# Performance work log

Measured on AMD Instinct MI355X. Metric: run time of the kernel, lower is better.

Reference implementation:

```python
import jax, jax.numpy as jnp
import numpy as np

N, D_IN, E, H, F, T = 50000, 128, 800000, 8, 32, 8
NEG_SLOPE = 0.2


def setup_inputs() -> dict:
    key = jax.random.key(0)
    ks = jax.random.split(key, 12)
    feat = jax.random.normal(ks[0], (N, D_IN), dtype=jnp.float32)
    edge_embeddings = jax.random.normal(ks[1], (E, H), dtype=jnp.float32)
    src = jax.random.randint(ks[2], (E,), 0, N, dtype=jnp.int32)
    dst = jnp.sort(jax.random.randint(ks[3], (E,), 0, N, dtype=jnp.int32))
    etype = jax.random.randint(ks[4], (E,), 0, T, dtype=jnp.int32)
    s = 0.05
    W_src = jax.random.normal(ks[5], (H * F, D_IN), dtype=jnp.float32) * s
    attn_l = jax.random.normal(ks[6], (1, H, F), dtype=jnp.float32) * s
    attn_r = jax.random.normal(ks[7], (1, H, F), dtype=jnp.float32) * s
    attn_e = jax.random.normal(ks[8], (1, H, F), dtype=jnp.float32) * s
    W_e = jax.random.normal(ks[9], (H * F, H), dtype=jnp.float32) * s
    type_emb = jax.random.normal(ks[10], (T, F), dtype=jnp.float32) * s
    k2 = jax.random.split(ks[11], 3)
    W_et = jax.random.normal(k2[0], (H * F, F), dtype=jnp.float32) * s
    attn_et = jax.random.normal(k2[1], (1, H, F), dtype=jnp.float32) * s
    bias = jnp.zeros((H * F,), dtype=jnp.float32)
    return dict(feat=feat, edge_embeddings=edge_embeddings, src=src, dst=dst,
                etype=etype, W_src=W_src, attn_l=attn_l, attn_r=attn_r,
                attn_e=attn_e, W_e=W_e, type_emb=type_emb, W_et=W_et,
                attn_et=attn_et, bias=bias)


def _leaky_relu(x):
    return jnp.where(x >= 0, x, NEG_SLOPE * x)


def reference(feat, edge_embeddings, src, dst, etype, W_src, attn_l, attn_r,
              attn_e, W_e, type_emb, W_et, attn_et, bias):
    n = feat.shape[0]
    # node transform (shared src/dst weights)
    fs = (feat @ W_src.T).reshape(n, H, F)           # [N,H,F]
    el = (fs * attn_l).sum(-1)                        # [N,H]
    er = (fs * attn_r).sum(-1)                        # [N,H]
    e = el[src] + er[dst]                             # [E,H] (u_add_v)
    # edge embedding attention term
    ee = (edge_embeddings @ W_e.T).reshape(-1, H, F)  # [E,H,F]
    e_score = (ee * attn_e).sum(-1)                   # [E,H]
    # edge type embedding attention term
    te = type_emb[etype]                              # [E,F]
    te = (te @ W_et.T).reshape(-1, H, F)              # [E,H,F]
    t_score = (te * attn_et).sum(-1)                  # [E,H]
    attn = e + e_score + t_score                      # attn_agg = sum
    # edge-type frequency normalization
    counts = jnp.bincount(etype, length=T).astype(jnp.float32)
    w = counts.sum() / (T * counts)                   # [T]
    attn = attn * w[etype][:, None]
    attn = _leaky_relu(attn)                          # v2=False -> after agg
    # edge softmax over incoming edges of each dst node
    m = jax.ops.segment_max(attn, dst, num_segments=n)  # [N,H]
    a = jnp.exp(attn - m[dst])
    z = jax.ops.segment_sum(a, dst, num_segments=n)     # [N,H]
    a = a / z[dst]                                      # [E,H]
    # weighted scatter aggregation
    msg = fs[src] * a[:, :, None]                       # [E,H,F]
    out = jax.ops.segment_sum(msg, dst, num_segments=n) # [N,H,F]
    return out + bias.reshape(1, H, F)
```

## Files before the change

kernel.cpp:

```cpp
#include <hip/hip_runtime.h>
#include <math.h>

#define N_NODES 50000
#define D_IN    128
#define E_EDGES 800000
#define H_HEADS 8
#define F_FEAT  32
#define T_TYPES 8
#define HF      256
#define NEG_SLOPE 0.2f
#define HIST_BLOCKS 64
#define GEMM_BLOCKS 391
#define OFF_BLOCKS  196
#define K1_HIST_BASE GEMM_BLOCKS
#define K1_OFF_BASE  (GEMM_BLOCKS + HIST_BLOCKS)
#define K1_TAB       (GEMM_BLOCKS + HIST_BLOCKS + OFF_BLOCKS)
#define K1_GRID      (K1_TAB + 1)
#define NGROUPS      ((N_NODES + 63) / 64)

using short8 = __attribute__((__ext_vector_type__(8))) short;
using f32x4  = __attribute__((__ext_vector_type__(4))) float;

__device__ inline float bf2f(unsigned short u) {
    union { unsigned int i; float f; } v; v.i = ((unsigned int)u) << 16; return v.f;
}
__device__ inline unsigned short f2bf(float f) {
    unsigned int x = __float_as_uint(f);
    unsigned int r = (x + 0x7fffu + ((x >> 16) & 1u)) >> 16;
    return (unsigned short)r;
}
__device__ inline unsigned int pk2bf(float a, float b) {
    return (unsigned int)f2bf(a) | ((unsigned int)f2bf(b) << 16);
}

__global__ __launch_bounds__(256) void prep_kernel(const float* __restrict__ feat,
                                                   const float* __restrict__ W,
                                                   const float* __restrict__ attn_l,
                                                   const float* __restrict__ attn_r,
                                                   const int*   __restrict__ etype,
                                                   const int*   __restrict__ dst,
                                                   const float* __restrict__ attn_e,
                                                   const float* __restrict__ W_e,
                                                   const float* __restrict__ attn_et,
                                                   const float* __restrict__ W_et,
                                                   const float* __restrict__ type_emb,
                                                   unsigned short* __restrict__ fsb,
                                                   float* __restrict__ el,
                                                   float* __restrict__ er,
                                                   int* __restrict__ partials,
                                                   int* __restrict__ off,
                                                   float* __restrict__ M,
                                                   float* __restrict__ ttab) {
    __shared__ unsigned short Wl[HF * D_IN];
    __shared__ int sw[4][8];
    __shared__ float q[8][32];
    const int t = threadIdx.x;

    if (blockIdx.x == K1_TAB) {
        {
            int h = t >> 5, f2 = t & 31;
            float s = 0.f;
#pragma unroll 8
            for (int f = 0; f < F_FEAT; ++f)
                s += attn_et[h * 32 + f] * W_et[(h * 32 + f) * 32 + f2];
            q[h][f2] = s;
        }
        __syncthreads();
        if (t < 64) {
            int h = t >> 3, j = t & 7;
            float m = 0.f;
#pragma unroll 8
            for (int f = 0; f < F_FEAT; ++f)
                m += attn_e[h * 32 + f] * W_e[(h * 32 + f) * 8 + j];
            M[h * 8 + j] = m;
            float tt = 0.f;
#pragma unroll 8
            for (int f2 = 0; f2 < F_FEAT; ++f2)
                tt += type_emb[j * 32 + f2] * q[h][f2];
            ttab[j * 8 + h] = tt;
        }
        return;
    }
    if (blockIdx.x >= K1_OFF_BASE) {
        int n = (blockIdx.x - K1_OFF_BASE) * 256 + t;
        if (n > N_NODES) return;
        int lo = 0, hi = E_EDGES;
        while (lo < hi) {
            int mid = (lo + hi) >> 1;
            if (dst[mid] < n) lo = mid + 1; else hi = mid;
        }
        off[n] = lo;
        return;
    }
    if (blockIdx.x >= K1_HIST_BASE) {
        const int hb = blockIdx.x - K1_HIST_BASE;
        int c[8] = {0,0,0,0,0,0,0,0};
        const int stride = HIST_BLOCKS * 256;
        for (int e = hb * 256 + t; e < E_EDGES; e += stride) {
            int ty = etype[e];
#pragma unroll
            for (int k = 0; k < 8; ++k) c[k] += (ty == k) ? 1 : 0;
        }
#pragma unroll
        for (int k = 0; k < 8; ++k) {
            c[k] += __shfl_xor(c[k], 1);  c[k] += __shfl_xor(c[k], 2);
            c[k] += __shfl_xor(c[k], 4);  c[k] += __shfl_xor(c[k], 8);
            c[k] += __shfl_xor(c[k], 16); c[k] += __shfl_xor(c[k], 32);
        }
        const int wv = t >> 6, l = t & 63;
        if (l == 0) {
#pragma unroll
            for (int k = 0; k < 8; ++k) sw[wv][k] = c[k];
        }
        __syncthreads();
        if (t < 8) partials[hb * 8 + t] = sw[0][t] + sw[1][t] + sw[2][t] + sw[3][t];
        return;
    }

    for (int i = 0; i < 16; ++i) {
        int slot = i * 256 + t;
        int n = slot >> 4, k16 = slot & 15;
        const float* wp = W + (size_t)n * D_IN + k16 * 8;
        float4 w0 = *(const float4*)wp;
        float4 w1 = *(const float4*)(wp + 4);
        union { unsigned int u[4]; short8 s; } ua;
        ua.u[0] = pk2bf(w0.x, w0.y); ua.u[1] = pk2bf(w0.z, w0.w);
        ua.u[2] = pk2bf(w1.x, w1.y); ua.u[3] = pk2bf(w1.z, w1.w);
        int idx = n * D_IN + ((k16 * 8) ^ ((n & 7) << 3));
        *(short8*)&Wl[idx] = ua.s;
    }
    __syncthreads();

    const int wid = t >> 6, l = t & 63;
    const int r16 = l & 15, kq = l >> 4;
    float alv0[8], alv1[8], arv0[8], arv1[8];
#pragma unroll
    for (int h = 0; h < 8; ++h) {
        alv0[h] = attn_l[h * 32 + r16];  alv1[h] = attn_l[h * 32 + 16 + r16];
        arv0[h] = attn_r[h * 32 + r16];  arv1[h] = attn_r[h * 32 + 16 + r16];
    }

    for (int grp = blockIdx.x; grp < NGROUPS; grp += GEMM_BLOCKS) {
        const int node0 = grp * 64 + wid * 16;
        int arow = node0 + r16;
        if (arow >= N_NODES) arow = N_NODES - 1;
        const float* fp = feat + (size_t)arow * D_IN + kq * 8;

        f32x4 acc[16];
#pragma unroll
        for (int i = 0; i < 16; ++i) acc[i] = (f32x4){0.f, 0.f, 0.f, 0.f};

#pragma unroll
        for (int kc = 0; kc < 4; ++kc) {
            float4 a0 = *(const float4*)(fp + kc * 32);
            float4 a1 = *(const float4*)(fp + kc * 32 + 4);
            union { unsigned int u[4]; short8 s; } ua;
            ua.u[0] = pk2bf(a0.x, a0.y); ua.u[1] = pk2bf(a0.z, a0.w);
            ua.u[2] = pk2bf(a1.x, a1.y); ua.u[3] = pk2bf(a1.z, a1.w);
            short8 af = ua.s;
#pragma unroll
            for (int nsub = 0; nsub < 16; ++nsub) {
                int n = nsub * 16 + r16;
                int idx = n * D_IN + ((kc * 32 + kq * 8) ^ ((n & 7) << 3));
                short8 bf = *(short8*)&Wl[idx];
                acc[nsub] = __builtin_amdgcn_mfma_f32_16x16x32_bf16(af, bf, acc[nsub], 0, 0, 0);
            }
        }

        const int nodeb = node0 + kq * 4;
#pragma unroll
        for (int h = 0; h < 8; ++h) {
            float ev[4], rv[4];
#pragma unroll
            for (int g = 0; g < 4; ++g) {
                ev[g] = acc[2 * h][g] * alv0[h] + acc[2 * h + 1][g] * alv1[h];
                rv[g] = acc[2 * h][g] * arv0[h] + acc[2 * h + 1][g] * arv1[h];
            }
#pragma unroll
            for (int g = 0; g < 4; ++g) {
                ev[g] += __shfl_xor(ev[g], 1); ev[g] += __shfl_xor(ev[g], 2);
                ev[g] += __shfl_xor(ev[g], 4); ev[g] += __shfl_xor(ev[g], 8);
                rv[g] += __shfl_xor(rv[g], 1); rv[g] += __shfl_xor(rv[g], 2);
                rv[g] += __shfl_xor(rv[g], 4); rv[g] += __shfl_xor(rv[g], 8);
            }
            if (r16 == 0) {
#pragma unroll
                for (int g = 0; g < 4; ++g) {
                    int nd = nodeb + g;
                    if (nd < N_NODES) {
                        el[nd * 8 + h] = ev[g];
                        er[nd * 8 + h] = rv[g];
                    }
                }
            }
        }
#pragma unroll
        for (int nsub = 0; nsub < 16; ++nsub) {
            int col = nsub * 16 + r16;
#pragma unroll
            for (int g = 0; g < 4; ++g) {
                int nd = nodeb + g;
                if (nd < N_NODES) fsb[(size_t)nd * HF + col] = f2bf(acc[nsub][g]);
            }
        }
    }
}

__global__ __launch_bounds__(256) void edge_kernel(const float* __restrict__ ee,
        const int* __restrict__ src, const int* __restrict__ dst,
        const int* __restrict__ etype, const float* __restrict__ el,
        const float* __restrict__ er, const float* __restrict__ M,
        const float* __restrict__ ttab, const int* __restrict__ partials,
        unsigned short* __restrict__ pexp) {
    __shared__ float sM[64], sT[64], sw[8];
    int t = threadIdx.x;
    if (t < 64) {
        sM[t] = M[t]; sT[t] = ttab[t];
        int j = t & 7, b = t >> 3;
        int c = 0;
#pragma unroll 8
        for (int i = 0; i < HIST_BLOCKS / 8; ++i)
            c += partials[(b + 8 * i) * 8 + j];
        c += __shfl_xor(c, 8); c += __shfl_xor(c, 16); c += __shfl_xor(c, 32);
        if (t < 8) {
            if (c < 1) c = 1;
            sw[t] = (float)E_EDGES / (8.0f * (float)c);
        }
    }
    __syncthreads();
    int e = blockIdx.x * 256 + t;
    if (e >= E_EDGES) return;
    int s = src[e], d = dst[e], ty = etype[e];
    float4 e0 = *(const float4*)&ee[(size_t)e * 8];
    float4 e1 = *(const float4*)&ee[(size_t)e * 8 + 4];
    float4 l0 = *(const float4*)&el[s * 8];
    float4 l1 = *(const float4*)&el[s * 8 + 4];
    float4 r0 = *(const float4*)&er[d * 8];
    float4 r1 = *(const float4*)&er[d * 8 + 4];
    float wt = sw[ty];
    float lv[8] = {l0.x,l0.y,l0.z,l0.w,l1.x,l1.y,l1.z,l1.w};
    float rv[8] = {r0.x,r0.y,r0.z,r0.w,r1.x,r1.y,r1.z,r1.w};
    unsigned int o[4];
#pragma unroll
    for (int hp = 0; hp < 4; ++hp) {
        float p2[2];
#pragma unroll
        for (int i = 0; i < 2; ++i) {
            int h = hp * 2 + i;
            float sc = lv[h] + rv[h] + sT[ty * 8 + h];
            sc += e0.x*sM[h*8+0] + e0.y*sM[h*8+1] + e0.z*sM[h*8+2] + e0.w*sM[h*8+3]
                + e1.x*sM[h*8+4] + e1.y*sM[h*8+5] + e1.z*sM[h*8+6] + e1.w*sM[h*8+7];
            sc *= wt;
            sc = (sc >= 0.f) ? sc : NEG_SLOPE * sc;
            p2[i] = __expf(sc);
        }
        o[hp] = (unsigned int)f2bf(p2[0]) | ((unsigned int)f2bf(p2[1]) << 16);
    }
    *(uint4*)&pexp[(size_t)e * 8] = make_uint4(o[0], o[1], o[2], o[3]);
}

__global__ __launch_bounds__(256) void agg_kernel(const unsigned short* __restrict__ pexp,
        const unsigned short* __restrict__ fsb, const int* __restrict__ src,
        const int* __restrict__ off, const float* __restrict__ bias,
        float* __restrict__ out) {
    __shared__ unsigned short plds[4][64][8];
    const int wid = threadIdx.x >> 6;
    const int l = threadIdx.x & 63;
    const int n = blockIdx.x * 4 + wid;
    if (n >= N_NODES) return;
    const int beg = off[n], end = off[n + 1];
    const int c0 = 4 * l;
    const int h = l >> 3;
    const float4 b4 = *(const float4*)&bias[c0];
    float* op = &out[(size_t)n * HF + c0];
    if (beg == end) { *(float4*)op = b4; return; }
    const unsigned short* mp = &plds[wid][0][0];
    float a0 = 0.f, a1 = 0.f, a2 = 0.f, a3 = 0.f, z = 0.f;
    for (int base = beg; base < end; base += 64) {
        const int remn = end - base;
        const int rem = remn < 64 ? remn : 64;
        int idx = base + l; if (idx >= end) idx = end - 1;
        const int sl = src[idx];
        {
            const uint4 pv = *(const uint4*)&pexp[(size_t)idx * 8];
            *(uint4*)&plds[wid][l][0] = pv;
        }
        int j = 0;
        for (; j + 4 <= rem; j += 4) {
            const int s0 = __shfl(sl, j),     s1 = __shfl(sl, j + 1);
            const int s2 = __shfl(sl, j + 2), s3 = __shfl(sl, j + 3);
            const float p0 = bf2f(mp[(j    ) * 8 + h]);
            const float p1 = bf2f(mp[(j + 1) * 8 + h]);
            const float p2 = bf2f(mp[(j + 2) * 8 + h]);
            const float p3 = bf2f(mp[(j + 3) * 8 + h]);
            const ushort4 f0 = *(const ushort4*)&fsb[(size_t)s0 * HF + c0];
            const ushort4 f1 = *(const ushort4*)&fsb[(size_t)s1 * HF + c0];
            const ushort4 f2 = *(const ushort4*)&fsb[(size_t)s2 * HF + c0];
            const ushort4 f3 = *(const ushort4*)&fsb[(size_t)s3 * HF + c0];
            a0 += p0 * bf2f(f0.x); a1 += p0 * bf2f(f0.y);
            a2 += p0 * bf2f(f0.z); a3 += p0 * bf2f(f0.w); z += p0;
            a0 += p1 * bf2f(f1.x); a1 += p1 * bf2f(f1.y);
            a2 += p1 * bf2f(f1.z); a3 += p1 * bf2f(f1.w); z += p1;
            a0 += p2 * bf2f(f2.x); a1 += p2 * bf2f(f2.y);
            a2 += p2 * bf2f(f2.z); a3 += p2 * bf2f(f2.w); z += p2;
            a0 += p3 * bf2f(f3.x); a1 += p3 * bf2f(f3.y);
            a2 += p3 * bf2f(f3.z); a3 += p3 * bf2f(f3.w); z += p3;
        }
        for (; j < rem; ++j) {
            const int s0 = __shfl(sl, j);
            const float p0 = bf2f(mp[j * 8 + h]);
            const ushort4 f0 = *(const ushort4*)&fsb[(size_t)s0 * HF + c0];
            a0 += p0 * bf2f(f0.x); a1 += p0 * bf2f(f0.y);
            a2 += p0 * bf2f(f0.z); a3 += p0 * bf2f(f0.w); z += p0;
        }
    }
    const float rz = 1.f / z;
    *(float4*)op = make_float4(a0 * rz + b4.x, a1 * rz + b4.y,
                               a2 * rz + b4.z, a3 * rz + b4.w);
}

extern "C" void kernel_launch(void* const* d_in, const int* in_sizes, int n_in,
                              void* d_out, int out_size, void* d_ws, size_t ws_size,
                              hipStream_t stream) {
    const float* feat     = (const float*)d_in[0];
    const float* ee       = (const float*)d_in[1];
    const int*   src      = (const int*)d_in[2];
    const int*   dst      = (const int*)d_in[3];
    const int*   etype    = (const int*)d_in[4];
    const float* W_src    = (const float*)d_in[5];
    const float* attn_l   = (const float*)d_in[6];
    const float* attn_r   = (const float*)d_in[7];
    const float* attn_e   = (const float*)d_in[8];
    const float* W_e      = (const float*)d_in[9];
    const float* type_emb = (const float*)d_in[10];
    const float* W_et     = (const float*)d_in[11];
    const float* attn_et  = (const float*)d_in[12];
    const float* bias     = (const float*)d_in[13];
    float* out = (float*)d_out;

    char* ws = (char*)d_ws;
    size_t o = 0;
    auto alloc = [&](size_t bytes) -> void* {
        void* p = ws + o;
        o = (o + bytes + 255) & ~(size_t)255;
        return p;
    };
    unsigned short* fsb  = (unsigned short*)alloc((size_t)N_NODES * HF * 2);
    unsigned short* pexp = (unsigned short*)alloc((size_t)E_EDGES * 8 * 2);
    float* el    = (float*)alloc((size_t)N_NODES * 8 * 4);
    float* er    = (float*)alloc((size_t)N_NODES * 8 * 4);
    int*   off   = (int*)alloc((size_t)(N_NODES + 1) * 4);
    int*   partials = (int*)alloc((size_t)HIST_BLOCKS * 8 * 4);
    float* M     = (float*)alloc(64 * 4);
    float* ttab  = (float*)alloc(64 * 4);

    prep_kernel<<<K1_GRID, 256, 0, stream>>>(feat, W_src, attn_l, attn_r,
                                             etype, dst, attn_e, W_e, attn_et,
                                             W_et, type_emb, fsb, el, er,
                                             partials, off, M, ttab);
    edge_kernel<<<(E_EDGES + 255) / 256, 256, 0, stream>>>(
        ee, src, dst, etype, el, er, M, ttab, partials, pexp);
    agg_kernel<<<(N_NODES + 3) / 4, 256, 0, stream>>>(pexp, fsb, src, off, bias, out);
}
```

Measured before the change: 105.8 us.

## Prefetch both node groups' features before W staging and share B fragments

Each GEMM block now handles exactly two 64-node groups at once. Both groups' feature rows are loaded before the weight matrix is converted into shared memory, so global load latency overlaps the weight staging. Each B fragment read from shared memory feeds two MFMAs, which halves LDS reads. The cost is much higher register pressure (32 accumulator vectors plus prefetched A data), which may lower occupancy. The hardcoded two-group assumption relies on NGROUPS being at most 2*GEMM_BLOCKS (782 <= 782).

```diff
diff --git a/kernel.cpp b/kernel.cpp
--- a/kernel.cpp
+++ b/kernel.cpp
@@ -32,6 +32,14 @@
 __device__ inline unsigned int pk2bf(float a, float b) {
     return (unsigned int)f2bf(a) | ((unsigned int)f2bf(b) << 16);
 }
+__device__ inline short8 cvt8(float4 a, float4 b) {
+    union { unsigned int u[4]; short8 s; } ua;
+    ua.u[0] = pk2bf(a.x, a.y); ua.u[1] = pk2bf(a.z, a.w);
+    ua.u[2] = pk2bf(b.x, b.y); ua.u[3] = pk2bf(b.z, b.w);
+    return ua.s;
+}
+
+#define MM(AF, BF, C) __builtin_amdgcn_mfma_f32_16x16x32_bf16((AF), (BF), (C), 0, 0, 0)
 
 __global__ __launch_bounds__(256) void prep_kernel(const float* __restrict__ feat,
                                                    const float* __restrict__ W,
@@ -117,22 +125,76 @@
         return;
     }
 
+    const int wid = t >> 6, l = t & 63;
+    const int r16 = l & 15, kq = l >> 4;
+    const int swz = (r16 & 7) << 3;
+    const int nodeA = blockIdx.x * 64 + wid * 16;
+    const int nodeB = (blockIdx.x + GEMM_BLOCKS) * 64 + wid * 16;
+    int arowA = nodeA + r16; if (arowA >= N_NODES) arowA = N_NODES - 1;
+    int arowB = nodeB + r16; if (arowB >= N_NODES) arowB = N_NODES - 1;
+    const float* fpA = feat + (size_t)arowA * D_IN + kq * 8;
+    const float* fpB = feat + (size_t)arowB * D_IN + kq * 8;
+    const float4 A0a = *(const float4*)(fpA +   0), A0b = *(const float4*)(fpA +   4);
+    const float4 A1a = *(const float4*)(fpA +  32), A1b = *(const float4*)(fpA +  36);
+    const float4 A2a = *(const float4*)(fpA +  64), A2b = *(const float4*)(fpA +  68);
+    const float4 A3a = *(const float4*)(fpA +  96), A3b = *(const float4*)(fpA + 100);
+    const float4 B0a = *(const float4*)(fpB +   0), B0b = *(const float4*)(fpB +   4);
+    const float4 B1a = *(const float4*)(fpB +  32), B1b = *(const float4*)(fpB +  36);
+    const float4 B2a = *(const float4*)(fpB +  64), B2b = *(const float4*)(fpB +  68);
+    const float4 B3a = *(const float4*)(fpB +  96), B3b = *(const float4*)(fpB + 100);
+
     for (int i = 0; i < 16; ++i) {
         int slot = i * 256 + t;
         int n = slot >> 4, k16 = slot & 15;
         const float* wp = W + (size_t)n * D_IN + k16 * 8;
         float4 w0 = *(const float4*)wp;
         float4 w1 = *(const float4*)(wp + 4);
-        union { unsigned int u[4]; short8 s; } ua;
-        ua.u[0] = pk2bf(w0.x, w0.y); ua.u[1] = pk2bf(w0.z, w0.w);
-        ua.u[2] = pk2bf(w1.x, w1.y); ua.u[3] = pk2bf(w1.z, w1.w);
         int idx = n * D_IN + ((k16 * 8) ^ ((n & 7) << 3));
-        *(short8*)&Wl[idx] = ua.s;
+        *(short8*)&Wl[idx] = cvt8(w0, w1);
     }
     __syncthreads();
 
-    const int wid = t >> 6, l = t & 63;
-    const int r16 = l & 15, kq = l >> 4;
+    const short8 afA0 = cvt8(A0a, A0b), afA1 = cvt8(A1a, A1b);
+    const short8 afA2 = cvt8(A2a, A2b), afA3 = cvt8(A3a, A3b);
+    const short8 afB0 = cvt8(B0a, B0b), afB1 = cvt8(B1a, B1b);
+    const short8 afB2 = cvt8(B2a, B2b), afB3 = cvt8(B3a, B3b);
+
+    f32x4 accA[16], accB[16];
+#pragma unroll
+    for (int i = 0; i < 16; ++i) {
+        accA[i] = (f32x4){0.f, 0.f, 0.f, 0.f};
+        accB[i] = (f32x4){0.f, 0.f, 0.f, 0.f};
+    }
+
+#define LDB(NS, KO) (*(const short8*)&Wl[((NS) * 16 + r16) * D_IN + ((KO) ^ swz)])
+#define KCBODY(KC, AFA, AFB) { \
+    const int KO = (KC) * 32 + kq * 8; \
+    short8 b0 = LDB(0,KO), b1 = LDB(1,KO), b2 = LDB(2,KO), b3 = LDB(3,KO); \
+    short8 b4 = LDB(4,KO), b5 = LDB(5,KO), b6 = LDB(6,KO), b7 = LDB(7,KO); \
+    accA[0] = MM(AFA, b0, accA[0]);  accB[0] = MM(AFB, b0, accB[0]); \
+    accA[1] = MM(AFA, b1, accA[1]);  accB[1] = MM(AFB, b1, accB[1]); \
+    accA[2] = MM(AFA, b2, accA[2]);  accB[2] = MM(AFB, b2, accB[2]); \
+    accA[3] = MM(AFA, b3, accA[3]);  accB[3] = MM(AFB, b3, accB[3]); \
+    accA[4] = MM(AFA, b4, accA[4]);  accB[4] = MM(AFB, b4, accB[4]); \
+    accA[5] = MM(AFA, b5, accA[5]);  accB[5] = MM(AFB, b5, accB[5]); \
+    accA[6] = MM(AFA, b6, accA[6]);  accB[6] = MM(AFB, b6, accB[6]); \
+    accA[7] = MM(AFA, b7, accA[7]);  accB[7] = MM(AFB, b7, accB[7]); \
+    b0 = LDB(8,KO);  b1 = LDB(9,KO);  b2 = LDB(10,KO); b3 = LDB(11,KO); \
+    b4 = LDB(12,KO); b5 = LDB(13,KO); b6 = LDB(14,KO); b7 = LDB(15,KO); \
+    accA[8]  = MM(AFA, b0, accA[8]);   accB[8]  = MM(AFB, b0, accB[8]); \
+    accA[9]  = MM(AFA, b1, accA[9]);   accB[9]  = MM(AFB, b1, accB[9]); \
+    accA[10] = MM(AFA, b2, accA[10]);  accB[10] = MM(AFB, b2, accB[10]); \
+    accA[11] = MM(AFA, b3, accA[11]);  accB[11] = MM(AFB, b3, accB[11]); \
+    accA[12] = MM(AFA, b4, accA[12]);  accB[12] = MM(AFB, b4, accB[12]); \
+    accA[13] = MM(AFA, b5, accA[13]);  accB[13] = MM(AFB, b5, accB[13]); \
+    accA[14] = MM(AFA, b6, accA[14]);  accB[14] = MM(AFB, b6, accB[14]); \
+    accA[15] = MM(AFA, b7, accA[15]);  accB[15] = MM(AFB, b7, accB[15]); }
+
+    KCBODY(0, afA0, afB0)
+    KCBODY(1, afA1, afB1)
+    KCBODY(2, afA2, afB2)
+    KCBODY(3, afA3, afB3)
+
     float alv0[8], alv1[8], arv0[8], arv1[8];
 #pragma unroll
     for (int h = 0; h < 8; ++h) {
@@ -140,33 +202,7 @@
         arv0[h] = attn_r[h * 32 + r16];  arv1[h] = attn_r[h * 32 + 16 + r16];
     }
 
-    for (int grp = blockIdx.x; grp < NGROUPS; grp += GEMM_BLOCKS) {
-        const int node0 = grp * 64 + wid * 16;
-        int arow = node0 + r16;
-        if (arow >= N_NODES) arow = N_NODES - 1;
-        const float* fp = feat + (size_t)arow * D_IN + kq * 8;
-
-        f32x4 acc[16];
-#pragma unroll
-        for (int i = 0; i < 16; ++i) acc[i] = (f32x4){0.f, 0.f, 0.f, 0.f};
-
-#pragma unroll
-        for (int kc = 0; kc < 4; ++kc) {
-            float4 a0 = *(const float4*)(fp + kc * 32);
-            float4 a1 = *(const float4*)(fp + kc * 32 + 4);
-            union { unsigned int u[4]; short8 s; } ua;
-            ua.u[0] = pk2bf(a0.x, a0.y); ua.u[1] = pk2bf(a0.z, a0.w);
-            ua.u[2] = pk2bf(a1.x, a1.y); ua.u[3] = pk2bf(a1.z, a1.w);
-            short8 af = ua.s;
-#pragma unroll
-            for (int nsub = 0; nsub < 16; ++nsub) {
-                int n = nsub * 16 + r16;
-                int idx = n * D_IN + ((kc * 32 + kq * 8) ^ ((n & 7) << 3));
-                short8 bf = *(short8*)&Wl[idx];
-                acc[nsub] = __builtin_amdgcn_mfma_f32_16x16x32_bf16(af, bf, acc[nsub], 0, 0, 0);
-            }
-        }
-
+    auto epilogue = [&](f32x4* acc, int node0) {
         const int nodeb = node0 + kq * 4;
 #pragma unroll
         for (int h = 0; h < 8; ++h) {
@@ -203,7 +239,9 @@
                 if (nd < N_NODES) fsb[(size_t)nd * HF + col] = f2bf(acc[nsub][g]);
             }
         }
-    }
+    };
+    epilogue(accA, nodeA);
+    epilogue(accB, nodeB);
 }
 
 __global__ __launch_bounds__(256) void edge_kernel(const float* __restrict__ ee,
```

Result: slower. 119.7 us (+13.2%).
